# Optimization experiments

Measured on AMD Instinct MI355X. Metric: run time of the kernel, lower is better.

The kernel has to match this reference:

```python
import jax, jax.numpy as jnp
import numpy as np

D = 50          # half-window
K = 2 * D + 1   # 101 window positions
P_SIZE = 100    # predictive-alignment hidden dim


def setup_inputs() -> dict:
    key = jax.random.key(0)
    ks = jax.random.split(key, 5)
    B, S, CQ, CC = 2, 2048, 256, 256
    q = jax.random.normal(ks[0], (B, S, CQ), jnp.float32)
    c_t = jax.random.normal(ks[1], (B, S, CC), jnp.float32)
    W_a = jax.random.normal(ks[2], (CC, CQ), jnp.float32) / np.sqrt(CQ).astype(np.float32)
    W_p = jax.random.normal(ks[3], (P_SIZE, CC), jnp.float32) / np.sqrt(CC).astype(np.float32)
    V_p = jax.random.normal(ks[4], (1, P_SIZE), jnp.float32) / np.sqrt(P_SIZE).astype(np.float32)
    return {"q": q, "c_t": c_t, "W_a": W_a, "W_p": W_p, "V_p": V_p}


def reference(q, c_t, W_a, W_p, V_p):
    B, S, CQ = q.shape
    # predictive alignment: p in (0, S), one predicted center per (b, s)
    p = S * jax.nn.sigmoid(jnp.tanh(c_t @ W_p.T) @ V_p.T)[..., 0]          # [B,S]
    offs = jnp.arange(-D, D + 1)                                           # [K]
    # torch .long() truncates toward zero (raw can be negative)
    raw = jnp.trunc(p[..., None] + offs[None, None, :] + 1.0).astype(jnp.int32)
    # clamp to [0, S+1] then mod (S+1): index 0 == padded (invalid) row,
    # matching torch's NaN-padded row 0 (S+1 wraps to 0 via the modulo)
    idx = jnp.clip(raw, 0, S + 1) % (S + 1)                                # [B,S,K]
    mask = idx == 0                                                        # invalid window slots
    # pad row 0 (torch pads with NaN then zeroes the NaN rows; we pad with 0
    # and mask by index -> identical math for finite q)
    q_pad = jnp.concatenate([jnp.zeros((B, 1, CQ), q.dtype), q], axis=1)   # [B,S+1,CQ]
    gathered = jnp.take_along_axis(q_pad, idx.reshape(B, S * K, 1), axis=1)
    q1 = jnp.where(mask[..., None], 0.0, gathered.reshape(B, S, K, CQ))    # [B,S,K,CQ]
    # score: W_a projection then dot with context
    Wq = jnp.einsum("bskq,cq->bskc", q1, W_a)                              # [B,S,K,CC]
    a = jnp.einsum("bskc,bsc->bsk", Wq, c_t)                               # [B,S,K]
    a = jnp.where(mask, -jnp.inf, a)
    attn = jax.nn.softmax(a, axis=2)                                       # [B,S,K]
    # gaussian decay centered at floor(p) (p > 0 so trunc == floor)
    exponent = -2.0 * (((offs[None, None, :] + jnp.trunc(p)[..., None] - p[..., None]) / D) ** 2)
    w = attn * jnp.exp(exponent)                                           # [B,S,K]
    s_t = jnp.einsum("bsk,bskc->bsc", w, q1)                               # [B,S,CQ]
    return s_t
```

## Files before the change

### kernel.cpp

```cpp
#include <hip/hip_runtime.h>
#include <math.h>

#define S_LEN 2048
#define NB    2
#define CQ_   256
#define CC_   256
#define DH    50
#define KW    101
#define PS    100
#define WTH   1e-5f

#define NB2   384
#define MT    64
#define NT    64
#define KC    32

__global__ __launch_bounds__(NB2) void k_prep(const float* __restrict__ Wa,
    const float* __restrict__ Wp, float* __restrict__ BT) {
  const int c = blockIdx.x, n = threadIdx.x;
  float v = 0.0f;
  if (n < CQ_)            v = Wa[(size_t)c * CQ_ + n];
  else if (n < CQ_ + PS)  v = Wp[(size_t)(n - CQ_) * CC_ + c];
  BT[(size_t)c * NB2 + n] = v;
}

__global__ __launch_bounds__(256) void k_gemm(const float* __restrict__ ct,
    const float* __restrict__ BT, float* __restrict__ G) {
  const int bm = blockIdx.x & 63;
  const int bn = blockIdx.x >> 6;
  const int r0 = bm * MT;
  const int n0 = bn * NT;
  const int tid = threadIdx.x;
  const int tx = tid & 15, ty = tid >> 4;

  __shared__ float As[KC][MT + 4];
  __shared__ float Bs[KC][NT + 4];

  float acc[4][4];
#pragma unroll
  for (int i = 0; i < 4; ++i)
#pragma unroll
    for (int j = 0; j < 4; ++j) acc[i][j] = 0.0f;

  const int kq = tid & 7,  mA = tid >> 3;
  const int nq = tid & 15, kB = tid >> 4;

  for (int c0 = 0; c0 < CC_; c0 += KC) {
    const float4 a0 = *(const float4*)&ct[(size_t)(r0 + mA) * CC_ + c0 + kq * 4];
    const float4 a1 = *(const float4*)&ct[(size_t)(r0 + mA + 32) * CC_ + c0 + kq * 4];
    const float4 b0 = *(const float4*)&BT[(size_t)(c0 + kB) * NB2 + n0 + nq * 4];
    const float4 b1 = *(const float4*)&BT[(size_t)(c0 + kB + 16) * NB2 + n0 + nq * 4];
    __syncthreads();
    As[kq * 4 + 0][mA] = a0.x;
    As[kq * 4 + 1][mA] = a0.y;
    As[kq * 4 + 2][mA] = a0.z;
    As[kq * 4 + 3][mA] = a0.w;
    As[kq * 4 + 0][mA + 32] = a1.x;
    As[kq * 4 + 1][mA + 32] = a1.y;
    As[kq * 4 + 2][mA + 32] = a1.z;
    As[kq * 4 + 3][mA + 32] = a1.w;
    *(float4*)&Bs[kB][nq * 4]      = b0;
    *(float4*)&Bs[kB + 16][nq * 4] = b1;
    __syncthreads();
#pragma unroll
    for (int k = 0; k < KC; ++k) {
      const float4 av = *(const float4*)&As[k][ty * 4];
      const float4 bv = *(const float4*)&Bs[k][tx * 4];
      const float a[4] = {av.x, av.y, av.z, av.w};
      const float b[4] = {bv.x, bv.y, bv.z, bv.w};
#pragma unroll
      for (int i = 0; i < 4; ++i)
#pragma unroll
        for (int j = 0; j < 4; ++j) acc[i][j] = fmaf(a[i], b[j], acc[i][j]);
    }
  }

#pragma unroll
  for (int i = 0; i < 4; ++i) {
    float4 o;
    o.x = acc[i][0]; o.y = acc[i][1]; o.z = acc[i][2]; o.w = acc[i][3];
    *(float4*)&G[(size_t)(r0 + ty * 4 + i) * NB2 + n0 + tx * 4] = o;
  }
}

__global__ __launch_bounds__(256) void k_p(const float* __restrict__ G,
    const float* __restrict__ Vp, float* __restrict__ p_out) {
  const int r = blockIdx.x * 256 + threadIdx.x;
  const float* h = G + (size_t)r * NB2 + CQ_;
  float H[PS];
#pragma unroll
  for (int j = 0; j < PS; j += 4) {
    const float4 v = *(const float4*)&h[j];
    H[j + 0] = v.x; H[j + 1] = v.y; H[j + 2] = v.z; H[j + 3] = v.w;
  }
  float s = 0.0f;
#pragma unroll
  for (int j = 0; j < PS; ++j) s += Vp[j] * tanhf(H[j]);
  p_out[r] = (float)S_LEN * (1.0f / (1.0f + expf(-s)));
}

__global__ __launch_bounds__(256, 4) void k_attn(const float* __restrict__ q,
    const float* __restrict__ p_in, const float* __restrict__ G,
    float* __restrict__ out) {
  const int wid  = threadIdx.x >> 6;
  const int row  = (blockIdx.x << 2) + wid;
  const int lane = threadIdx.x & 63;
  const int b    = row >> 11;

  __shared__ float ss[4][128];
  __shared__ float sw[4][128];

  const float p  = p_in[row];
  const float tp = truncf(p);
  const float* qb = q + (size_t)b * S_LEN * CQ_;

  const int sub = lane >> 4;
  const int cb  = (lane & 15) * 16;

  const float* vrow = G + (size_t)row * NB2 + cb;
  const float4 v0 = *(const float4*)(vrow);
  const float4 v1 = *(const float4*)(vrow + 4);
  const float4 v2 = *(const float4*)(vrow + 8);
  const float4 v3 = *(const float4*)(vrow + 12);

  if (lane >= KW - 64) ss[wid][64 + lane] = -INFINITY;

  for (int g = 0; g < 26; g += 2) {
    const int ka = (g << 2) + sub;
    const int kb = ka + 4;
    const float ta = p + (float)(ka - DH) + 1.0f;
    const float tb = p + (float)(kb - DH) + 1.0f;
    const int rawa = (int)ta;
    const int rawb = (int)tb;
    const bool oka = (rawa >= 1) && (rawa <= S_LEN) && (ka < KW);
    const bool okb = (rawb >= 1) && (rawb <= S_LEN) && (kb < KW);
    const float* qra = qb + (size_t)(oka ? rawa - 1 : 0) * CQ_ + cb;
    const float* qrb = qb + (size_t)(okb ? rawb - 1 : 0) * CQ_ + cb;

    const float4 a0 = *(const float4*)(qra);
    const float4 a1 = *(const float4*)(qra + 4);
    const float4 a2 = *(const float4*)(qra + 8);
    const float4 a3 = *(const float4*)(qra + 12);
    const float4 b0 = *(const float4*)(qrb);
    const float4 b1 = *(const float4*)(qrb + 4);
    const float4 b2 = *(const float4*)(qrb + 8);
    const float4 b3 = *(const float4*)(qrb + 12);

    float t0 = a0.x * v0.x, t1 = a1.x * v1.x, t2 = a2.x * v2.x, t3 = a3.x * v3.x;
    t0 = fmaf(a0.y, v0.y, t0); t1 = fmaf(a1.y, v1.y, t1);
    t2 = fmaf(a2.y, v2.y, t2); t3 = fmaf(a3.y, v3.y, t3);
    t0 = fmaf(a0.z, v0.z, t0); t1 = fmaf(a1.z, v1.z, t1);
    t2 = fmaf(a2.z, v2.z, t2); t3 = fmaf(a3.z, v3.z, t3);
    t0 = fmaf(a0.w, v0.w, t0); t1 = fmaf(a1.w, v1.w, t1);
    t2 = fmaf(a2.w, v2.w, t2); t3 = fmaf(a3.w, v3.w, t3);
    float sA = (t0 + t1) + (t2 + t3);
    sA += __shfl_xor(sA, 1, 64);
    sA += __shfl_xor(sA, 2, 64);
    sA += __shfl_xor(sA, 4, 64);
    sA += __shfl_xor(sA, 8, 64);
    sA = oka ? sA : -INFINITY;
    if ((lane & 15) == 0) ss[wid][ka] = sA;

    float u0 = b0.x * v0.x, u1 = b1.x * v1.x, u2 = b2.x * v2.x, u3 = b3.x * v3.x;
    u0 = fmaf(b0.y, v0.y, u0); u1 = fmaf(b1.y, v1.y, u1);
    u2 = fmaf(b2.y, v2.y, u2); u3 = fmaf(b3.y, v3.y, u3);
    u0 = fmaf(b0.z, v0.z, u0); u1 = fmaf(b1.z, v1.z, u1);
    u2 = fmaf(b2.z, v2.z, u2); u3 = fmaf(b3.z, v3.z, u3);
    u0 = fmaf(b0.w, v0.w, u0); u1 = fmaf(b1.w, v1.w, u1);
    u2 = fmaf(b2.w, v2.w, u2); u3 = fmaf(b3.w, v3.w, u3);
    float sB = (u0 + u1) + (u2 + u3);
    sB += __shfl_xor(sB, 1, 64);
    sB += __shfl_xor(sB, 2, 64);
    sB += __shfl_xor(sB, 4, 64);
    sB += __shfl_xor(sB, 8, 64);
    sB = okb ? sB : -INFINITY;
    if ((lane & 15) == 0) ss[wid][kb] = sB;
  }

  const float s0 = ss[wid][lane];
  const float s1 = ss[wid][64 + lane];

  float m = fmaxf(s0, s1);
#pragma unroll
  for (int off = 1; off < 64; off <<= 1) m = fmaxf(m, __shfl_xor(m, off, 64));

  const float e0 = __expf(s0 - m);
  const float e1 = __expf(s1 - m);
  float den = e0 + e1;
#pragma unroll
  for (int off = 1; off < 64; off <<= 1) den += __shfl_xor(den, off, 64);
  const float inv = 1.0f / den;

  float g0 = ((float)(lane - DH) + tp - p) / (float)DH;
  float g1 = ((float)(lane + (64 - DH)) + tp - p) / (float)DH;
  const float w0 = e0 * __expf(-2.0f * g0 * g0) * inv;
  const float w1 = e1 * __expf(-2.0f * g1 * g1) * inv;
  sw[wid][lane] = w0;
  if (lane < KW - 64) sw[wid][64 + lane] = w1;

  unsigned long long m0 = __ballot(w0 > WTH);
  unsigned long long m1 = __ballot((lane < KW - 64) && (w1 > WTH));

  float4 acc = make_float4(0.0f, 0.0f, 0.0f, 0.0f);
  while ((m0 | m1) != 0ull) {
    int kk[4];
#pragma unroll
    for (int i = 0; i < 4; ++i) {
      int k = -1;
      if (m0)      { k = __builtin_ctzll(m0);      m0 &= m0 - 1; }
      else if (m1) { k = 64 + __builtin_ctzll(m1); m1 &= m1 - 1; }
      kk[i] = k;
    }
#pragma unroll
    for (int i = 0; i < 4; ++i) {
      if (kk[i] >= 0) {
        const float wk = sw[wid][kk[i]];
        const float t = p + (float)(kk[i] - DH) + 1.0f;
        const int r = (int)t - 1;
        const float4 qv = *(const float4*)(qb + (size_t)r * CQ_ + lane * 4);
        acc.x = fmaf(wk, qv.x, acc.x);
        acc.y = fmaf(wk, qv.y, acc.y);
        acc.z = fmaf(wk, qv.z, acc.z);
        acc.w = fmaf(wk, qv.w, acc.w);
      }
    }
  }
  *(float4*)(out + (size_t)row * CQ_ + lane * 4) = acc;
}

extern "C" void kernel_launch(void* const* d_in, const int* in_sizes, int n_in,
                              void* d_out, int out_size, void* d_ws, size_t ws_size,
                              hipStream_t stream) {
  const float* q  = (const float*)d_in[0];
  const float* ct = (const float*)d_in[1];
  const float* Wa = (const float*)d_in[2];
  const float* Wp = (const float*)d_in[3];
  const float* Vp = (const float*)d_in[4];
  float* out = (float*)d_out;

  float* ws    = (float*)d_ws;
  float* p_ws  = ws;
  float* BT_ws = ws + NB * S_LEN;
  float* G_ws  = BT_ws + (size_t)CC_ * NB2;

  k_prep<<<CC_, NB2, 0, stream>>>(Wa, Wp, BT_ws);
  k_gemm<<<64 * 6, 256, 0, stream>>>(ct, BT_ws, G_ws);
  k_p   <<<(NB * S_LEN) / 256, 256, 0, stream>>>(G_ws, Vp, p_ws);
  k_attn<<<(NB * S_LEN) / 4, 256, 0, stream>>>(q, p_ws, G_ws, out);
}
```

Measured before the change: 125.4 us.

## Split each attention row across four waves and shrink GEMM tiles

The attention kernel now assigns one block of four waves to each output row instead of one wave per row. The waves share the 101 window scores through shared memory, split the weighted-sum gather round-robin, and combine their partials with a shared-memory reduction. The GEMM tile shrinks from 64 to 32 rows so the grid has twice as many blocks. This is meant to raise parallelism and latency hiding, at the cost of extra block syncs, a shared reduction and less register reuse per thread in the GEMM.

Result: slower. 129.3 us (+3.1%).

```diff
diff --git a/kernel.cpp b/kernel.cpp
--- a/kernel.cpp
+++ b/kernel.cpp
@@ -11,7 +11,7 @@
 #define WTH   1e-5f
 
 #define NB2   384
-#define MT    64
+#define MT    32
 #define NT    64
 #define KC    32
 
@@ -26,28 +26,26 @@
 
 __global__ __launch_bounds__(256) void k_gemm(const float* __restrict__ ct,
     const float* __restrict__ BT, float* __restrict__ G) {
-  const int bm = blockIdx.x & 63;
-  const int bn = blockIdx.x >> 6;
+  const int bm = blockIdx.x & 127;
+  const int bn = blockIdx.x >> 7;
   const int r0 = bm * MT;
   const int n0 = bn * NT;
   const int tid = threadIdx.x;
-  const int tx = tid & 15, ty = tid >> 4;
+  const int tx = tid & 31;
+  const int ty = tid >> 5;
 
   __shared__ float As[KC][MT + 4];
   __shared__ float Bs[KC][NT + 4];
 
-  float acc[4][4];
-#pragma unroll
-  for (int i = 0; i < 4; ++i)
-#pragma unroll
-    for (int j = 0; j < 4; ++j) acc[i][j] = 0.0f;
+  float acc[4][2];
+#pragma unroll
+  for (int i = 0; i < 4; ++i) { acc[i][0] = 0.0f; acc[i][1] = 0.0f; }
 
   const int kq = tid & 7,  mA = tid >> 3;
   const int nq = tid & 15, kB = tid >> 4;
 
   for (int c0 = 0; c0 < CC_; c0 += KC) {
     const float4 a0 = *(const float4*)&ct[(size_t)(r0 + mA) * CC_ + c0 + kq * 4];
-    const float4 a1 = *(const float4*)&ct[(size_t)(r0 + mA + 32) * CC_ + c0 + kq * 4];
     const float4 b0 = *(const float4*)&BT[(size_t)(c0 + kB) * NB2 + n0 + nq * 4];
     const float4 b1 = *(const float4*)&BT[(size_t)(c0 + kB + 16) * NB2 + n0 + nq * 4];
     __syncthreads();
@@ -55,31 +53,28 @@
     As[kq * 4 + 1][mA] = a0.y;
     As[kq * 4 + 2][mA] = a0.z;
     As[kq * 4 + 3][mA] = a0.w;
-    As[kq * 4 + 0][mA + 32] = a1.x;
-    As[kq * 4 + 1][mA + 32] = a1.y;
-    As[kq * 4 + 2][mA + 32] = a1.z;
-    As[kq * 4 + 3][mA + 32] = a1.w;
     *(float4*)&Bs[kB][nq * 4]      = b0;
     *(float4*)&Bs[kB + 16][nq * 4] = b1;
     __syncthreads();
 #pragma unroll
     for (int k = 0; k < KC; ++k) {
       const float4 av = *(const float4*)&As[k][ty * 4];
-      const float4 bv = *(const float4*)&Bs[k][tx * 4];
-      const float a[4] = {av.x, av.y, av.z, av.w};
-      const float b[4] = {bv.x, bv.y, bv.z, bv.w};
-#pragma unroll
-      for (int i = 0; i < 4; ++i)
-#pragma unroll
-        for (int j = 0; j < 4; ++j) acc[i][j] = fmaf(a[i], b[j], acc[i][j]);
+      const float2 bv = *(const float2*)&Bs[k][tx * 2];
+      acc[0][0] = fmaf(av.x, bv.x, acc[0][0]);
+      acc[0][1] = fmaf(av.x, bv.y, acc[0][1]);
+      acc[1][0] = fmaf(av.y, bv.x, acc[1][0]);
+      acc[1][1] = fmaf(av.y, bv.y, acc[1][1]);
+      acc[2][0] = fmaf(av.z, bv.x, acc[2][0]);
+      acc[2][1] = fmaf(av.z, bv.y, acc[2][1]);
+      acc[3][0] = fmaf(av.w, bv.x, acc[3][0]);
+      acc[3][1] = fmaf(av.w, bv.y, acc[3][1]);
     }
   }
 
 #pragma unroll
   for (int i = 0; i < 4; ++i) {
-    float4 o;
-    o.x = acc[i][0]; o.y = acc[i][1]; o.z = acc[i][2]; o.w = acc[i][3];
-    *(float4*)&G[(size_t)(r0 + ty * 4 + i) * NB2 + n0 + tx * 4] = o;
+    float2 o; o.x = acc[i][0]; o.y = acc[i][1];
+    *(float2*)&G[(size_t)(r0 + ty * 4 + i) * NB2 + n0 + tx * 2] = o;
   }
 }
 
@@ -99,16 +94,17 @@
   p_out[r] = (float)S_LEN * (1.0f / (1.0f + expf(-s)));
 }
 
-__global__ __launch_bounds__(256, 4) void k_attn(const float* __restrict__ q,
+__global__ __launch_bounds__(256, 6) void k_attn(const float* __restrict__ q,
     const float* __restrict__ p_in, const float* __restrict__ G,
     float* __restrict__ out) {
-  const int wid  = threadIdx.x >> 6;
-  const int row  = (blockIdx.x << 2) + wid;
-  const int lane = threadIdx.x & 63;
+  const int row  = blockIdx.x;
+  const int tid  = threadIdx.x;
+  const int wid  = tid >> 6;
+  const int lane = tid & 63;
   const int b    = row >> 11;
 
-  __shared__ float ss[4][128];
-  __shared__ float sw[4][128];
+  __shared__ float ss[128];
+  __shared__ float sacc[4][CQ_];
 
   const float p  = p_in[row];
   const float tp = truncf(p);
@@ -123,67 +119,42 @@
   const float4 v2 = *(const float4*)(vrow + 8);
   const float4 v3 = *(const float4*)(vrow + 12);
 
-  if (lane >= KW - 64) ss[wid][64 + lane] = -INFINITY;
-
-  for (int g = 0; g < 26; g += 2) {
-    const int ka = (g << 2) + sub;
-    const int kb = ka + 4;
-    const float ta = p + (float)(ka - DH) + 1.0f;
-    const float tb = p + (float)(kb - DH) + 1.0f;
-    const int rawa = (int)ta;
-    const int rawb = (int)tb;
-    const bool oka = (rawa >= 1) && (rawa <= S_LEN) && (ka < KW);
-    const bool okb = (rawb >= 1) && (rawb <= S_LEN) && (kb < KW);
-    const float* qra = qb + (size_t)(oka ? rawa - 1 : 0) * CQ_ + cb;
-    const float* qrb = qb + (size_t)(okb ? rawb - 1 : 0) * CQ_ + cb;
-
-    const float4 a0 = *(const float4*)(qra);
-    const float4 a1 = *(const float4*)(qra + 4);
-    const float4 a2 = *(const float4*)(qra + 8);
-    const float4 a3 = *(const float4*)(qra + 12);
-    const float4 b0 = *(const float4*)(qrb);
-    const float4 b1 = *(const float4*)(qrb + 4);
-    const float4 b2 = *(const float4*)(qrb + 8);
-    const float4 b3 = *(const float4*)(qrb + 12);
-
-    float t0 = a0.x * v0.x, t1 = a1.x * v1.x, t2 = a2.x * v2.x, t3 = a3.x * v3.x;
-    t0 = fmaf(a0.y, v0.y, t0); t1 = fmaf(a1.y, v1.y, t1);
-    t2 = fmaf(a2.y, v2.y, t2); t3 = fmaf(a3.y, v3.y, t3);
-    t0 = fmaf(a0.z, v0.z, t0); t1 = fmaf(a1.z, v1.z, t1);
-    t2 = fmaf(a2.z, v2.z, t2); t3 = fmaf(a3.z, v3.z, t3);
-    t0 = fmaf(a0.w, v0.w, t0); t1 = fmaf(a1.w, v1.w, t1);
-    t2 = fmaf(a2.w, v2.w, t2); t3 = fmaf(a3.w, v3.w, t3);
-    float sA = (t0 + t1) + (t2 + t3);
-    sA += __shfl_xor(sA, 1, 64);
-    sA += __shfl_xor(sA, 2, 64);
-    sA += __shfl_xor(sA, 4, 64);
-    sA += __shfl_xor(sA, 8, 64);
-    sA = oka ? sA : -INFINITY;
-    if ((lane & 15) == 0) ss[wid][ka] = sA;
-
-    float u0 = b0.x * v0.x, u1 = b1.x * v1.x, u2 = b2.x * v2.x, u3 = b3.x * v3.x;
-    u0 = fmaf(b0.y, v0.y, u0); u1 = fmaf(b1.y, v1.y, u1);
-    u2 = fmaf(b2.y, v2.y, u2); u3 = fmaf(b3.y, v3.y, u3);
-    u0 = fmaf(b0.z, v0.z, u0); u1 = fmaf(b1.z, v1.z, u1);
-    u2 = fmaf(b2.z, v2.z, u2); u3 = fmaf(b3.z, v3.z, u3);
-    u0 = fmaf(b0.w, v0.w, u0); u1 = fmaf(b1.w, v1.w, u1);
-    u2 = fmaf(b2.w, v2.w, u2); u3 = fmaf(b3.w, v3.w, u3);
-    float sB = (u0 + u1) + (u2 + u3);
-    sB += __shfl_xor(sB, 1, 64);
-    sB += __shfl_xor(sB, 2, 64);
-    sB += __shfl_xor(sB, 4, 64);
-    sB += __shfl_xor(sB, 8, 64);
-    sB = okb ? sB : -INFINITY;
-    if ((lane & 15) == 0) ss[wid][kb] = sB;
-  }
-
-  const float s0 = ss[wid][lane];
-  const float s1 = ss[wid][64 + lane];
-
+  if (tid >= KW && tid < 128) ss[tid] = -INFINITY;
+
+#pragma unroll
+  for (int step = 0; step < 7; ++step) {
+    const int k = 16 * step + 4 * sub + wid;
+    const float t = p + (float)(k - DH) + 1.0f;
+    const int raw = (int)t;
+    const bool ok = (raw >= 1) && (raw <= S_LEN) && (k < KW);
+    const float* qr = qb + (size_t)(ok ? raw - 1 : 0) * CQ_ + cb;
+    const float4 q0 = *(const float4*)(qr);
+    const float4 q1 = *(const float4*)(qr + 4);
+    const float4 q2 = *(const float4*)(qr + 8);
+    const float4 q3 = *(const float4*)(qr + 12);
+
+    float t0 = q0.x * v0.x, t1 = q1.x * v1.x, t2 = q2.x * v2.x, t3 = q3.x * v3.x;
+    t0 = fmaf(q0.y, v0.y, t0); t1 = fmaf(q1.y, v1.y, t1);
+    t2 = fmaf(q2.y, v2.y, t2); t3 = fmaf(q3.y, v3.y, t3);
+    t0 = fmaf(q0.z, v0.z, t0); t1 = fmaf(q1.z, v1.z, t1);
+    t2 = fmaf(q2.z, v2.z, t2); t3 = fmaf(q3.z, v3.z, t3);
+    t0 = fmaf(q0.w, v0.w, t0); t1 = fmaf(q1.w, v1.w, t1);
+    t2 = fmaf(q2.w, v2.w, t2); t3 = fmaf(q3.w, v3.w, t3);
+    float s = (t0 + t1) + (t2 + t3);
+    s += __shfl_xor(s, 1, 64);
+    s += __shfl_xor(s, 2, 64);
+    s += __shfl_xor(s, 4, 64);
+    s += __shfl_xor(s, 8, 64);
+    s = ok ? s : -INFINITY;
+    if ((lane & 15) == 0) ss[k] = s;
+  }
+  __syncthreads();
+
+  const float s0 = ss[lane];
+  const float s1 = ss[64 + lane];
   float m = fmaxf(s0, s1);
 #pragma unroll
   for (int off = 1; off < 64; off <<= 1) m = fmaxf(m, __shfl_xor(m, off, 64));
-
   const float e0 = __expf(s0 - m);
   const float e1 = __expf(s1 - m);
   float den = e0 + e1;
@@ -195,37 +166,47 @@
   float g1 = ((float)(lane + (64 - DH)) + tp - p) / (float)DH;
   const float w0 = e0 * __expf(-2.0f * g0 * g0) * inv;
   const float w1 = e1 * __expf(-2.0f * g1 * g1) * inv;
-  sw[wid][lane] = w0;
-  if (lane < KW - 64) sw[wid][64 + lane] = w1;
 
   unsigned long long m0 = __ballot(w0 > WTH);
   unsigned long long m1 = __ballot((lane < KW - 64) && (w1 > WTH));
 
   float4 acc = make_float4(0.0f, 0.0f, 0.0f, 0.0f);
-  while ((m0 | m1) != 0ull) {
-    int kk[4];
-#pragma unroll
-    for (int i = 0; i < 4; ++i) {
-      int k = -1;
-      if (m0)      { k = __builtin_ctzll(m0);      m0 &= m0 - 1; }
-      else if (m1) { k = 64 + __builtin_ctzll(m1); m1 &= m1 - 1; }
-      kk[i] = k;
+  int i = 0;
+  while (m0) {
+    const int k = __builtin_ctzll(m0);
+    m0 &= m0 - 1;
+    if ((i & 3) == wid) {
+      const float wk = __shfl(w0, k, 64);
+      const float t = p + (float)(k - DH) + 1.0f;
+      const int r = (int)t - 1;
+      const float4 qv = *(const float4*)(qb + (size_t)r * CQ_ + lane * 4);
+      acc.x = fmaf(wk, qv.x, acc.x);
+      acc.y = fmaf(wk, qv.y, acc.y);
+      acc.z = fmaf(wk, qv.z, acc.z);
+      acc.w = fmaf(wk, qv.w, acc.w);
     }
-#pragma unroll
-    for (int i = 0; i < 4; ++i) {
-      if (kk[i] >= 0) {
-        const float wk = sw[wid][kk[i]];
-        const float t = p + (float)(kk[i] - DH) + 1.0f;
-        const int r = (int)t - 1;
-        const float4 qv = *(const float4*)(qb + (size_t)r * CQ_ + lane * 4);
-        acc.x = fmaf(wk, qv.x, acc.x);
-        acc.y = fmaf(wk, qv.y, acc.y);
-        acc.z = fmaf(wk, qv.z, acc.z);
-        acc.w = fmaf(wk, qv.w, acc.w);
-      }
+    ++i;
+  }
+  while (m1) {
+    const int k64 = __builtin_ctzll(m1);
+    m1 &= m1 - 1;
+    if ((i & 3) == wid) {
+      const float wk = __shfl(w1, k64, 64);
+      const float t = p + (float)(k64 + (64 - DH)) + 1.0f;
+      const int r = (int)t - 1;
+      const float4 qv = *(const float4*)(qb + (size_t)r * CQ_ + lane * 4);
+      acc.x = fmaf(wk, qv.x, acc.x);
+      acc.y = fmaf(wk, qv.y, acc.y);
+      acc.z = fmaf(wk, qv.z, acc.z);
+      acc.w = fmaf(wk, qv.w, acc.w);
     }
-  }
-  *(float4*)(out + (size_t)row * CQ_ + lane * 4) = acc;
+    ++i;
+  }
+  *(float4*)&sacc[wid][lane * 4] = acc;
+  __syncthreads();
+
+  const float r = ((sacc[0][tid] + sacc[1][tid]) + (sacc[2][tid] + sacc[3][tid]));
+  out[(size_t)row * CQ_ + tid] = r;
 }
 
 extern "C" void kernel_launch(void* const* d_in, const int* in_sizes, int n_in,
@@ -244,7 +225,7 @@
   float* G_ws  = BT_ws + (size_t)CC_ * NB2;
 
   k_prep<<<CC_, NB2, 0, stream>>>(Wa, Wp, BT_ws);
-  k_gemm<<<64 * 6, 256, 0, stream>>>(ct, BT_ws, G_ws);
+  k_gemm<<<128 * 6, 256, 0, stream>>>(ct, BT_ws, G_ws);
   k_p   <<<(NB * S_LEN) / 256, 256, 0, stream>>>(G_ws, Vp, p_ws);
-  k_attn<<<(NB * S_LEN) / 4, 256, 0, stream>>>(q, p_ws, G_ws, out);
-}
+  k_attn<<<NB * S_LEN, 256, 0, stream>>>(q, p_ws, G_ws, out);
+}
```

## Split GEMM reduction dimension in two, widen attention score loads

Applied to the files above, without the earlier changes.

The projection GEMM now splits its 256-long reduction into two halves, launching twice as many blocks (768). Each half writes a partial result buffer, and the consumers (k_p and k_attn) add the two partials when they read them. The attention score loop also batches four window rows per iteration and switches to a strided per-lane column layout, so more loads are in flight and accesses coalesce better. The cost is extra workspace, twice the reads of G, and higher register pressure in k_attn.

Measured after the change: 118.8 us. 5.3% less time.

```diff
diff --git a/kernel.cpp b/kernel.cpp
--- a/kernel.cpp
+++ b/kernel.cpp
@@ -14,6 +14,7 @@
 #define MT    64
 #define NT    64
 #define KC    32
+#define HOFF  ((size_t)4096 * NB2)
 
 __global__ __launch_bounds__(NB2) void k_prep(const float* __restrict__ Wa,
     const float* __restrict__ Wp, float* __restrict__ BT) {
@@ -24,10 +25,13 @@
   BT[(size_t)c * NB2 + n] = v;
 }
 
-__global__ __launch_bounds__(256) void k_gemm(const float* __restrict__ ct,
+__global__ __launch_bounds__(256, 3) void k_gemm(const float* __restrict__ ct,
     const float* __restrict__ BT, float* __restrict__ G) {
-  const int bm = blockIdx.x & 63;
-  const int bn = blockIdx.x >> 6;
+  const int x  = blockIdx.x;
+  const int kh = (x >= 384) ? 1 : 0;
+  const int t  = x - kh * 384;
+  const int bm = t & 63;
+  const int bn = t >> 6;
   const int r0 = bm * MT;
   const int n0 = bn * NT;
   const int tid = threadIdx.x;
@@ -45,7 +49,8 @@
   const int kq = tid & 7,  mA = tid >> 3;
   const int nq = tid & 15, kB = tid >> 4;
 
-  for (int c0 = 0; c0 < CC_; c0 += KC) {
+  const int c0base = kh * 128;
+  for (int c0 = c0base; c0 < c0base + 128; c0 += KC) {
     const float4 a0 = *(const float4*)&ct[(size_t)(r0 + mA) * CC_ + c0 + kq * 4];
     const float4 a1 = *(const float4*)&ct[(size_t)(r0 + mA + 32) * CC_ + c0 + kq * 4];
     const float4 b0 = *(const float4*)&BT[(size_t)(c0 + kB) * NB2 + n0 + nq * 4];
@@ -75,23 +80,27 @@
     }
   }
 
+  float* Gh = G + (size_t)kh * HOFF;
 #pragma unroll
   for (int i = 0; i < 4; ++i) {
     float4 o;
     o.x = acc[i][0]; o.y = acc[i][1]; o.z = acc[i][2]; o.w = acc[i][3];
-    *(float4*)&G[(size_t)(r0 + ty * 4 + i) * NB2 + n0 + tx * 4] = o;
+    *(float4*)&Gh[(size_t)(r0 + ty * 4 + i) * NB2 + n0 + tx * 4] = o;
   }
 }
 
 __global__ __launch_bounds__(256) void k_p(const float* __restrict__ G,
     const float* __restrict__ Vp, float* __restrict__ p_out) {
   const int r = blockIdx.x * 256 + threadIdx.x;
-  const float* h = G + (size_t)r * NB2 + CQ_;
+  const float* h0 = G + (size_t)r * NB2 + CQ_;
+  const float* h1 = G + HOFF + (size_t)r * NB2 + CQ_;
   float H[PS];
 #pragma unroll
   for (int j = 0; j < PS; j += 4) {
-    const float4 v = *(const float4*)&h[j];
-    H[j + 0] = v.x; H[j + 1] = v.y; H[j + 2] = v.z; H[j + 3] = v.w;
+    const float4 a = *(const float4*)&h0[j];
+    const float4 b = *(const float4*)&h1[j];
+    H[j + 0] = a.x + b.x; H[j + 1] = a.y + b.y;
+    H[j + 2] = a.z + b.z; H[j + 3] = a.w + b.w;
   }
   float s = 0.0f;
 #pragma unroll
@@ -115,66 +124,64 @@
   const float* qb = q + (size_t)b * S_LEN * CQ_;
 
   const int sub = lane >> 4;
-  const int cb  = (lane & 15) * 16;
-
-  const float* vrow = G + (size_t)row * NB2 + cb;
-  const float4 v0 = *(const float4*)(vrow);
-  const float4 v1 = *(const float4*)(vrow + 4);
-  const float4 v2 = *(const float4*)(vrow + 8);
-  const float4 v3 = *(const float4*)(vrow + 12);
+  const int sl  = lane & 15;
+  const int c4  = sl * 4;
+
+  const float* vr0 = G + (size_t)row * NB2;
+  const float* vr1 = G + HOFF + (size_t)row * NB2;
+  float4 v0, v1, v2, v3;
+  {
+    const float4 x0 = *(const float4*)(vr0 + c4);
+    const float4 x1 = *(const float4*)(vr0 + 64 + c4);
+    const float4 x2 = *(const float4*)(vr0 + 128 + c4);
+    const float4 x3 = *(const float4*)(vr0 + 192 + c4);
+    const float4 y0 = *(const float4*)(vr1 + c4);
+    const float4 y1 = *(const float4*)(vr1 + 64 + c4);
+    const float4 y2 = *(const float4*)(vr1 + 128 + c4);
+    const float4 y3 = *(const float4*)(vr1 + 192 + c4);
+    v0.x = x0.x + y0.x; v0.y = x0.y + y0.y; v0.z = x0.z + y0.z; v0.w = x0.w + y0.w;
+    v1.x = x1.x + y1.x; v1.y = x1.y + y1.y; v1.z = x1.z + y1.z; v1.w = x1.w + y1.w;
+    v2.x = x2.x + y2.x; v2.y = x2.y + y2.y; v2.z = x2.z + y2.z; v2.w = x2.w + y2.w;
+    v3.x = x3.x + y3.x; v3.y = x3.y + y3.y; v3.z = x3.z + y3.z; v3.w = x3.w + y3.w;
+  }
 
   if (lane >= KW - 64) ss[wid][64 + lane] = -INFINITY;
 
-  for (int g = 0; g < 26; g += 2) {
-    const int ka = (g << 2) + sub;
-    const int kb = ka + 4;
-    const float ta = p + (float)(ka - DH) + 1.0f;
-    const float tb = p + (float)(kb - DH) + 1.0f;
-    const int rawa = (int)ta;
-    const int rawb = (int)tb;
-    const bool oka = (rawa >= 1) && (rawa <= S_LEN) && (ka < KW);
-    const bool okb = (rawb >= 1) && (rawb <= S_LEN) && (kb < KW);
-    const float* qra = qb + (size_t)(oka ? rawa - 1 : 0) * CQ_ + cb;
-    const float* qrb = qb + (size_t)(okb ? rawb - 1 : 0) * CQ_ + cb;
-
-    const float4 a0 = *(const float4*)(qra);
-    const float4 a1 = *(const float4*)(qra + 4);
-    const float4 a2 = *(const float4*)(qra + 8);
-    const float4 a3 = *(const float4*)(qra + 12);
-    const float4 b0 = *(const float4*)(qrb);
-    const float4 b1 = *(const float4*)(qrb + 4);
-    const float4 b2 = *(const float4*)(qrb + 8);
-    const float4 b3 = *(const float4*)(qrb + 12);
-
-    float t0 = a0.x * v0.x, t1 = a1.x * v1.x, t2 = a2.x * v2.x, t3 = a3.x * v3.x;
-    t0 = fmaf(a0.y, v0.y, t0); t1 = fmaf(a1.y, v1.y, t1);
-    t2 = fmaf(a2.y, v2.y, t2); t3 = fmaf(a3.y, v3.y, t3);
-    t0 = fmaf(a0.z, v0.z, t0); t1 = fmaf(a1.z, v1.z, t1);
-    t2 = fmaf(a2.z, v2.z, t2); t3 = fmaf(a3.z, v3.z, t3);
-    t0 = fmaf(a0.w, v0.w, t0); t1 = fmaf(a1.w, v1.w, t1);
-    t2 = fmaf(a2.w, v2.w, t2); t3 = fmaf(a3.w, v3.w, t3);
-    float sA = (t0 + t1) + (t2 + t3);
-    sA += __shfl_xor(sA, 1, 64);
-    sA += __shfl_xor(sA, 2, 64);
-    sA += __shfl_xor(sA, 4, 64);
-    sA += __shfl_xor(sA, 8, 64);
-    sA = oka ? sA : -INFINITY;
-    if ((lane & 15) == 0) ss[wid][ka] = sA;
-
-    float u0 = b0.x * v0.x, u1 = b1.x * v1.x, u2 = b2.x * v2.x, u3 = b3.x * v3.x;
-    u0 = fmaf(b0.y, v0.y, u0); u1 = fmaf(b1.y, v1.y, u1);
-    u2 = fmaf(b2.y, v2.y, u2); u3 = fmaf(b3.y, v3.y, u3);
-    u0 = fmaf(b0.z, v0.z, u0); u1 = fmaf(b1.z, v1.z, u1);
-    u2 = fmaf(b2.z, v2.z, u2); u3 = fmaf(b3.z, v3.z, u3);
-    u0 = fmaf(b0.w, v0.w, u0); u1 = fmaf(b1.w, v1.w, u1);
-    u2 = fmaf(b2.w, v2.w, u2); u3 = fmaf(b3.w, v3.w, u3);
-    float sB = (u0 + u1) + (u2 + u3);
-    sB += __shfl_xor(sB, 1, 64);
-    sB += __shfl_xor(sB, 2, 64);
-    sB += __shfl_xor(sB, 4, 64);
-    sB += __shfl_xor(sB, 8, 64);
-    sB = okb ? sB : -INFINITY;
-    if ((lane & 15) == 0) ss[wid][kb] = sB;
+  for (int g = 0; g < 26; g += 4) {
+    int   kk4[4];
+    bool  ok4[4];
+    float4 Q[4][4];
+#pragma unroll
+    for (int i = 0; i < 4; ++i) {
+      const int k = ((g + i) << 2) + sub;
+      const float t = p + (float)(k - DH) + 1.0f;
+      const int raw = (int)t;
+      const bool ok = (raw >= 1) && (raw <= S_LEN) && (k < KW);
+      kk4[i] = k; ok4[i] = ok;
+      const float* qr = qb + (size_t)(ok ? raw - 1 : 0) * CQ_;
+      Q[i][0] = *(const float4*)(qr + c4);
+      Q[i][1] = *(const float4*)(qr + 64 + c4);
+      Q[i][2] = *(const float4*)(qr + 128 + c4);
+      Q[i][3] = *(const float4*)(qr + 192 + c4);
+    }
+#pragma unroll
+    for (int i = 0; i < 4; ++i) {
+      float t0 = Q[i][0].x * v0.x, t1 = Q[i][1].x * v1.x;
+      float t2 = Q[i][2].x * v2.x, t3 = Q[i][3].x * v3.x;
+      t0 = fmaf(Q[i][0].y, v0.y, t0); t1 = fmaf(Q[i][1].y, v1.y, t1);
+      t2 = fmaf(Q[i][2].y, v2.y, t2); t3 = fmaf(Q[i][3].y, v3.y, t3);
+      t0 = fmaf(Q[i][0].z, v0.z, t0); t1 = fmaf(Q[i][1].z, v1.z, t1);
+      t2 = fmaf(Q[i][2].z, v2.z, t2); t3 = fmaf(Q[i][3].z, v3.z, t3);
+      t0 = fmaf(Q[i][0].w, v0.w, t0); t1 = fmaf(Q[i][1].w, v1.w, t1);
+      t2 = fmaf(Q[i][2].w, v2.w, t2); t3 = fmaf(Q[i][3].w, v3.w, t3);
+      float s = (t0 + t1) + (t2 + t3);
+      s += __shfl_xor(s, 1, 64);
+      s += __shfl_xor(s, 2, 64);
+      s += __shfl_xor(s, 4, 64);
+      s += __shfl_xor(s, 8, 64);
+      s = ok4[i] ? s : -INFINITY;
+      if (sl == 0) ss[wid][kk4[i]] = s;
+    }
   }
 
   const float s0 = ss[wid][lane];
@@ -244,7 +251,7 @@
   float* G_ws  = BT_ws + (size_t)CC_ * NB2;
 
   k_prep<<<CC_, NB2, 0, stream>>>(Wa, Wp, BT_ws);
-  k_gemm<<<64 * 6, 256, 0, stream>>>(ct, BT_ws, G_ws);
+  k_gemm<<<768, 256, 0, stream>>>(ct, BT_ws, G_ws);
   k_p   <<<(NB * S_LEN) / 256, 256, 0, stream>>>(G_ws, Vp, p_ws);
   k_attn<<<(NB * S_LEN) / 4, 256, 0, stream>>>(q, p_ws, G_ws, out);
 }
```
